# Optimization experiments

Measured on AMD Instinct MI355X. Metric: run time of the kernel, lower is better.

Reference implementation:

```python
import jax, jax.numpy as jnp
import numpy as np

FEATURES = 8
MAX_LAG = 50
OMEGA, ALPHA, BETA = 0.05, 0.1, 0.85   # garch_params
NU = 4.0                               # Student-t dof (hardcoded in source)
W_ACL, W_GARCH = 10.0, 0.001           # loss_weights
LOG_2PI = float(np.log(2.0 * np.pi))


def setup_inputs() -> dict:
    key = jax.random.key(0)
    k1, k2 = jax.random.split(key)
    x_true = jax.random.normal(k1, (4096, 512, FEATURES), dtype=jnp.float32)
    dec_out = jax.random.normal(k2, (4096, 512, 2 * FEATURES), dtype=jnp.float32)
    return {"x_true": x_true, "dec_out": dec_out}


def _series(y_pred):
    # concat(seq 0 full series, last value of every other sequence) -> [T + B - 1]
    return jnp.concatenate([y_pred[0, :, 0], y_pred[1:, -1, 0]], axis=0)


def _acl_loss(y_pred):
    s = _series(y_pred)
    n = s.shape[0]
    sc = s - jnp.mean(s)
    fft_len = 2 * n
    F = jnp.fft.rfft(sc, n=fft_len)
    autocorr = jnp.fft.irfft(jnp.conj(F) * F, n=fft_len)  # real by construction
    variance = jnp.sum(jnp.square(sc))
    autocorr = autocorr[: MAX_LAG + 1] / variance
    return jnp.mean(jnp.square(autocorr[1:]))


def _garch_nll_loss(y_pred):
    s = _series(y_pred)
    r = s - jnp.mean(s)
    r2 = jnp.square(r)
    sigma0 = OMEGA / (1.0 - ALPHA - BETA)  # unconditional variance

    def step(prev_sigma_sq, cur_r2):
        new = OMEGA + ALPHA * cur_r2 + BETA * prev_sigma_sq
        return new, new

    _, cond_var = jax.lax.scan(step, sigma0, r2)
    scale = jnp.sqrt(cond_var * (NU - 2.0) / NU)
    z = r / scale
    # StudentT(df=NU, loc=0, scale).log_prob(r)
    lp = (jax.scipy.special.gammaln((NU + 1.0) / 2.0)
          - jax.scipy.special.gammaln(NU / 2.0)
          - 0.5 * jnp.log(NU * jnp.pi)
          - jnp.log(scale)
          - (NU + 1.0) / 2.0 * jnp.log1p(z * z / NU))
    return -jnp.sum(lp)


def _gaussian_nll(x_true, dec_out):
    mean = dec_out[..., :FEATURES]
    log_var = dec_out[..., FEATURES:]
    ll = -0.5 * (LOG_2PI + log_var + jnp.square(x_true - mean) * jnp.exp(-log_var))
    return -jnp.mean(jnp.sum(ll, axis=(1, 2)))


def reference(x_true, dec_out):
    y_pred = dec_out[..., :FEATURES]  # generated_x = decoder means
    recon = _gaussian_nll(x_true, dec_out)
    acl = _acl_loss(y_pred)
    garch = _garch_nll_loss(y_pred)
    return recon + W_ACL * acl + W_GARCH * garch
```

## Files before the change

### kernel.cpp

```cpp
#include <hip/hip_runtime.h>

#define NS        4607
#define NBLK1     8192
#define N_TOTAL   16777216.0

#define WS_PART   0
#define WS_SRAW   8192
#define WS_GARCH  (8192 + NS)
#define WS_ACLSUM (8192 + NS + 1)
#define WS_CNT    (8192 + NS + 2)

__device__ __forceinline__ float wave_sum(float v) {
    for (int o = 32; o > 0; o >>= 1) v += __shfl_down(v, o);
    return v;
}

__global__ __launch_bounds__(256) void recon_kernel(
    const float* __restrict__ x, const float* __restrict__ dec,
    float* __restrict__ ws)
{
    const int tid = threadIdx.x;
    const long long pixBase = (long long)blockIdx.x * 256;
    const float4* dec4 = (const float4*)(dec + pixBase * 16);
    const float4* x4   = (const float4*)(x + pixBase * 8);

    float4 dv[4], xv[4];
#pragma unroll
    for (int r = 0; r < 4; ++r) {
        const int w = tid + r * 256;
        dv[r] = dec4[w];
        const int u = ((w >> 2) << 1) | (w & 1);
        xv[r] = x4[u];
    }

    float acc = 0.f;
#pragma unroll
    for (int r = 0; r < 4; ++r) {
        const int w = tid + r * 256;
        const int q = w & 3;
        float4 a = dv[r], b;
        b.x = __shfl_xor(a.x, 2);
        b.y = __shfl_xor(a.y, 2);
        b.z = __shfl_xor(a.z, 2);
        b.w = __shfl_xor(a.w, 2);
        const bool im = (q < 2);
        float4 m, lv;
        m.x  = im ? a.x : b.x;  m.y  = im ? a.y : b.y;
        m.z  = im ? a.z : b.z;  m.w  = im ? a.w : b.w;
        lv.x = im ? b.x : a.x;  lv.y = im ? b.y : a.y;
        lv.z = im ? b.z : a.z;  lv.w = im ? b.w : a.w;
        float4 xx = xv[r];
        float d;
        d = xx.x - m.x; acc += lv.x + d * d * __expf(-lv.x);
        d = xx.y - m.y; acc += lv.y + d * d * __expf(-lv.y);
        d = xx.z - m.z; acc += lv.z + d * d * __expf(-lv.z);
        d = xx.w - m.w; acc += lv.w + d * d * __expf(-lv.w);

        if (q == 0) {
            const long long pix = pixBase + (w >> 2);
            if (pix < 512)               ws[WS_SRAW + (int)pix] = m.x;
            else if ((pix & 511) == 511) ws[WS_SRAW + (int)(pix >> 9) + 511] = m.x;
        }
    }

    acc = wave_sum(acc);
    __shared__ float s4[4];
    if ((tid & 63) == 0) s4[tid >> 6] = acc;
    __syncthreads();
    if (tid == 0) {
        ws[WS_PART + blockIdx.x] = 0.5f * (s4[0] + s4[1] + s4[2] + s4[3]);
        if (blockIdx.x == 0) {
            ws[WS_GARCH]  = 0.f;
            ws[WS_ACLSUM] = 0.f;
            ((int*)ws)[WS_CNT] = 0;
        }
    }
}

__global__ __launch_bounds__(256) void tail_kernel(float* __restrict__ ws,
                                                   float* __restrict__ out)
{
    const float OMEGA = 0.05f, ALPHA = 0.1f, BETA = 0.85f;
    const int tid  = threadIdx.x;
    const int lane = tid & 63;
    const int wv   = tid >> 6;

    __shared__ float sc[NS];
    __shared__ float s4[4];
    __shared__ int   isLast;

    float lsum = 0.f;
    for (int j = tid; j < NS; j += 256) { float v = ws[WS_SRAW + j]; sc[j] = v; lsum += v; }
    lsum = wave_sum(lsum);
    __syncthreads();
    if (lane == 0) s4[wv] = lsum;
    __syncthreads();
    const float mean = (s4[0] + s4[1] + s4[2] + s4[3]) / (float)NS;

    float vsum = 0.f;
    __syncthreads();
    for (int j = tid; j < NS; j += 256) { float v = sc[j] - mean; sc[j] = v; vsum += v * v; }
    vsum = wave_sum(vsum);
    __syncthreads();
    if (lane == 0) s4[wv] = vsum;
    __syncthreads();
    const float var = s4[0] + s4[1] + s4[2] + s4[3];

    if (blockIdx.x == 0) {
        const int start = tid * 18;
        const int end   = min(start + 18, NS);
        float e = 0.f, p = 1.f;
        for (int i = start; i < end; ++i) {
            float r2 = sc[i] * sc[i];
            e = (OMEGA + ALPHA * r2) + BETA * e;
            p *= BETA;
        }
        for (int o = 1; o < 64; o <<= 1) {
            float pe = __shfl_up(e, o), pp = __shfl_up(p, o);
            if (lane >= o) { e = e + p * pe; p = p * pp; }
        }
        __shared__ float wE[4], wP[4];
        if (lane == 63) { wE[wv] = e; wP[wv] = p; }
        __syncthreads();
        float cE = 0.f, cP = 1.f;
        for (int t = 0; t < wv; ++t) { cE = wE[t] + wP[t] * cE; cP = wP[t] * cP; }
        float eE = __shfl_up(e, 1), eP = __shfl_up(p, 1);
        if (lane == 0) { eE = 0.f; eP = 1.f; }
        float prev = (eE + eP * cE) + (eP * cP) * 1.0f;
        float g = 0.f;
        for (int i = start; i < end; ++i) {
            float r2 = sc[i] * sc[i];
            float cv = OMEGA + ALPHA * r2 + BETA * prev;
            prev = cv;
            g += 0.5f * logf(0.5f * cv) + 2.5f * log1pf(r2 / (2.f * cv));
        }
        g = wave_sum(g);
        __syncthreads();
        if (lane == 0) s4[wv] = g;
        __syncthreads();
        if (tid == 0) atomicAdd(&ws[WS_GARCH], s4[0] + s4[1] + s4[2] + s4[3]);
    } else {
        const int k = blockIdx.x;
        float a = 0.f;
        for (int i = tid; i < NS - k; i += 256) a += sc[i] * sc[i + k];
        a = wave_sum(a);
        __syncthreads();
        if (lane == 0) s4[wv] = a;
        __syncthreads();
        if (tid == 0) {
            float r = (s4[0] + s4[1] + s4[2] + s4[3]) / var;
            atomicAdd(&ws[WS_ACLSUM], r * r);
        }
    }

    __syncthreads();
    if (tid == 0) {
        __threadfence();
        isLast = (atomicAdd((int*)ws + WS_CNT, 1) == 50) ? 1 : 0;
    }
    __syncthreads();
    if (isLast) {
        __threadfence();
        __shared__ double d4[4];
        double ds = 0.0;
        for (int i = tid; i < NBLK1; i += 256) ds += (double)ws[WS_PART + i];
        for (int o = 32; o > 0; o >>= 1) ds += __shfl_down(ds, o);
        if (lane == 0) d4[wv] = ds;
        __syncthreads();
        if (tid == 0) {
            float garch_f = atomicAdd(&ws[WS_GARCH], 0.f);
            float acl_f   = atomicAdd(&ws[WS_ACLSUM], 0.f);
            const double LOG_2PI = 1.8378770664093453;
            const double NEG_C   = 0.9808292530117262;
            double q = d4[0] + d4[1] + d4[2] + d4[3];
            double recon = 0.5 * (q + N_TOTAL * LOG_2PI) / 4096.0;
            double acl   = (double)acl_f / 50.0;
            double garch = (double)garch_f + (double)NS * NEG_C;
            out[0] = (float)(recon + 10.0 * acl + 0.001 * garch);
        }
    }
}

extern "C" void kernel_launch(void* const* d_in, const int* in_sizes, int n_in,
                              void* d_out, int out_size, void* d_ws, size_t ws_size,
                              hipStream_t stream) {
    const float* x_true  = (const float*)d_in[0];
    const float* dec_out = (const float*)d_in[1];
    float* ws  = (float*)d_ws;
    float* out = (float*)d_out;

    recon_kernel<<<NBLK1, 256, 0, stream>>>(x_true, dec_out, ws);
    tail_kernel<<<51, 256, 0, stream>>>(ws, out);
}
```

Before: 251.4 us.

## Overlap ACL/GARCH tail work with recon blocks in one merged kernel

Merges the serial tail blocks (autocorrelation lags and GARCH scan) into the recon kernel as the first 51 blocks. These blocks read the series values straight from dec_out, so they run alongside the bandwidth-bound recon reduction instead of after it. A small single-block final kernel then combines the per-block partials, replacing the atomic counter and last-block pattern. The cost is that each of the 51 tail blocks does strided gathers from global memory and uses large shared memory, which can reduce occupancy early in the grid.

```diff
diff --git a/kernel.cpp b/kernel.cpp
--- a/kernel.cpp
+++ b/kernel.cpp
@@ -1,183 +1,176 @@
 #include <hip/hip_runtime.h>
 
 #define NS        4607
-#define NBLK1     8192
+#define NRECON    8192
+#define NTAIL     51
 #define N_TOTAL   16777216.0
 
 #define WS_PART   0
-#define WS_SRAW   8192
-#define WS_GARCH  (8192 + NS)
-#define WS_ACLSUM (8192 + NS + 1)
-#define WS_CNT    (8192 + NS + 2)
+#define WS_GARCH  8192
+#define WS_ACL    8193
 
 __device__ __forceinline__ float wave_sum(float v) {
     for (int o = 32; o > 0; o >>= 1) v += __shfl_down(v, o);
     return v;
 }
 
-__global__ __launch_bounds__(256) void recon_kernel(
+__global__ __launch_bounds__(256) void main_kernel(
     const float* __restrict__ x, const float* __restrict__ dec,
     float* __restrict__ ws)
 {
-    const int tid = threadIdx.x;
-    const long long pixBase = (long long)blockIdx.x * 256;
-    const float4* dec4 = (const float4*)(dec + pixBase * 16);
-    const float4* x4   = (const float4*)(x + pixBase * 8);
+    const int tid  = threadIdx.x;
+    const int lane = tid & 63;
+    const int wv   = tid >> 6;
 
-    float4 dv[4], xv[4];
+    if (blockIdx.x >= NTAIL) {
+        const int tile = blockIdx.x - NTAIL;
+        const long long pixBase = (long long)tile * 256;
+        const float4* dec4 = (const float4*)(dec + pixBase * 16);
+        const float4* x4   = (const float4*)(x + pixBase * 8);
+
+        float4 dv[4], xv[4];
 #pragma unroll
-    for (int r = 0; r < 4; ++r) {
-        const int w = tid + r * 256;
-        dv[r] = dec4[w];
-        const int u = ((w >> 2) << 1) | (w & 1);
-        xv[r] = x4[u];
-    }
+        for (int r = 0; r < 4; ++r) {
+            const int w = tid + r * 256;
+            dv[r] = dec4[w];
+            const int u = ((w >> 2) << 1) | (w & 1);
+            xv[r] = x4[u];
+        }
 
-    float acc = 0.f;
+        float acc = 0.f;
 #pragma unroll
-    for (int r = 0; r < 4; ++r) {
-        const int w = tid + r * 256;
-        const int q = w & 3;
-        float4 a = dv[r], b;
-        b.x = __shfl_xor(a.x, 2);
-        b.y = __shfl_xor(a.y, 2);
-        b.z = __shfl_xor(a.z, 2);
-        b.w = __shfl_xor(a.w, 2);
-        const bool im = (q < 2);
-        float4 m, lv;
-        m.x  = im ? a.x : b.x;  m.y  = im ? a.y : b.y;
-        m.z  = im ? a.z : b.z;  m.w  = im ? a.w : b.w;
-        lv.x = im ? b.x : a.x;  lv.y = im ? b.y : a.y;
-        lv.z = im ? b.z : a.z;  lv.w = im ? b.w : a.w;
-        float4 xx = xv[r];
-        float d;
-        d = xx.x - m.x; acc += lv.x + d * d * __expf(-lv.x);
-        d = xx.y - m.y; acc += lv.y + d * d * __expf(-lv.y);
-        d = xx.z - m.z; acc += lv.z + d * d * __expf(-lv.z);
-        d = xx.w - m.w; acc += lv.w + d * d * __expf(-lv.w);
+        for (int r = 0; r < 4; ++r) {
+            const int w = tid + r * 256;
+            const int q = w & 3;
+            float4 a = dv[r], b;
+            b.x = __shfl_xor(a.x, 2);
+            b.y = __shfl_xor(a.y, 2);
+            b.z = __shfl_xor(a.z, 2);
+            b.w = __shfl_xor(a.w, 2);
+            const bool im = (q < 2);
+            float4 m, lv;
+            m.x  = im ? a.x : b.x;  m.y  = im ? a.y : b.y;
+            m.z  = im ? a.z : b.z;  m.w  = im ? a.w : b.w;
+            lv.x = im ? b.x : a.x;  lv.y = im ? b.y : a.y;
+            lv.z = im ? b.z : a.z;  lv.w = im ? b.w : a.w;
+            float4 xx = xv[r];
+            float d;
+            d = xx.x - m.x; acc += lv.x + d * d * __expf(-lv.x);
+            d = xx.y - m.y; acc += lv.y + d * d * __expf(-lv.y);
+            d = xx.z - m.z; acc += lv.z + d * d * __expf(-lv.z);
+            d = xx.w - m.w; acc += lv.w + d * d * __expf(-lv.w);
+        }
 
-        if (q == 0) {
-            const long long pix = pixBase + (w >> 2);
-            if (pix < 512)               ws[WS_SRAW + (int)pix] = m.x;
-            else if ((pix & 511) == 511) ws[WS_SRAW + (int)(pix >> 9) + 511] = m.x;
+        acc = wave_sum(acc);
+        __shared__ float p4[4];
+        if (lane == 0) p4[wv] = acc;
+        __syncthreads();
+        if (tid == 0) ws[WS_PART + tile] = 0.5f * (p4[0] + p4[1] + p4[2] + p4[3]);
+    } else {
+        const float OMEGA = 0.05f, ALPHA = 0.1f, BETA = 0.85f;
+        __shared__ float sc[NS];
+        __shared__ float s4[4];
+
+        float lsum = 0.f;
+        for (int j = tid; j < NS; j += 256) {
+            float v = (j < 512) ? dec[(long long)j * 16]
+                                : dec[(long long)(j - 511) * 8192 + 8176];
+            sc[j] = v;
+            lsum += v;
         }
-    }
+        lsum = wave_sum(lsum);
+        __syncthreads();
+        if (lane == 0) s4[wv] = lsum;
+        __syncthreads();
+        const float mean = (s4[0] + s4[1] + s4[2] + s4[3]) / (float)NS;
 
-    acc = wave_sum(acc);
-    __shared__ float s4[4];
-    if ((tid & 63) == 0) s4[tid >> 6] = acc;
-    __syncthreads();
-    if (tid == 0) {
-        ws[WS_PART + blockIdx.x] = 0.5f * (s4[0] + s4[1] + s4[2] + s4[3]);
+        float vsum = 0.f;
+        __syncthreads();
+        for (int j = tid; j < NS; j += 256) { float v = sc[j] - mean; sc[j] = v; vsum += v * v; }
+        vsum = wave_sum(vsum);
+        __syncthreads();
+        if (lane == 0) s4[wv] = vsum;
+        __syncthreads();
+        const float var = s4[0] + s4[1] + s4[2] + s4[3];
+
         if (blockIdx.x == 0) {
-            ws[WS_GARCH]  = 0.f;
-            ws[WS_ACLSUM] = 0.f;
-            ((int*)ws)[WS_CNT] = 0;
+            const int start = tid * 18;
+            const int end   = min(start + 18, NS);
+            float e = 0.f, p = 1.f;
+            for (int i = start; i < end; ++i) {
+                float r2 = sc[i] * sc[i];
+                e = (OMEGA + ALPHA * r2) + BETA * e;
+                p *= BETA;
+            }
+            for (int o = 1; o < 64; o <<= 1) {
+                float pe = __shfl_up(e, o), pp = __shfl_up(p, o);
+                if (lane >= o) { e = e + p * pe; p = p * pp; }
+            }
+            __shared__ float wE[4], wP[4];
+            if (lane == 63) { wE[wv] = e; wP[wv] = p; }
+            __syncthreads();
+            float cE = 0.f, cP = 1.f;
+            for (int t = 0; t < wv; ++t) { cE = wE[t] + wP[t] * cE; cP = wP[t] * cP; }
+            float eE = __shfl_up(e, 1), eP = __shfl_up(p, 1);
+            if (lane == 0) { eE = 0.f; eP = 1.f; }
+            float prev = (eE + eP * cE) + (eP * cP) * 1.0f;
+            float g = 0.f;
+            for (int i = start; i < end; ++i) {
+                float r2 = sc[i] * sc[i];
+                float cv = OMEGA + ALPHA * r2 + BETA * prev;
+                prev = cv;
+                g += 0.5f * logf(0.5f * cv) + 2.5f * log1pf(r2 / (2.f * cv));
+            }
+            g = wave_sum(g);
+            __syncthreads();
+            if (lane == 0) s4[wv] = g;
+            __syncthreads();
+            if (tid == 0) ws[WS_GARCH] = s4[0] + s4[1] + s4[2] + s4[3];
+        } else {
+            const int k = blockIdx.x;
+            float a = 0.f;
+            for (int i = tid; i < NS - k; i += 256) a += sc[i] * sc[i + k];
+            a = wave_sum(a);
+            __syncthreads();
+            if (lane == 0) s4[wv] = a;
+            __syncthreads();
+            if (tid == 0) {
+                float r = (s4[0] + s4[1] + s4[2] + s4[3]) / var;
+                ws[WS_ACL + (k - 1)] = r * r;
+            }
         }
     }
 }
 
-__global__ __launch_bounds__(256) void tail_kernel(float* __restrict__ ws,
-                                                   float* __restrict__ out)
+__global__ __launch_bounds__(256) void final_kernel(
+    const float* __restrict__ ws, float* __restrict__ out)
 {
-    const float OMEGA = 0.05f, ALPHA = 0.1f, BETA = 0.85f;
     const int tid  = threadIdx.x;
     const int lane = tid & 63;
     const int wv   = tid >> 6;
+    __shared__ double d4[4];
+    __shared__ float  aclbuf[1];
 
-    __shared__ float sc[NS];
-    __shared__ float s4[4];
-    __shared__ int   isLast;
+    double ds = 0.0;
+    for (int i = tid; i < NRECON; i += 256) ds += (double)ws[WS_PART + i];
+    for (int o = 32; o > 0; o >>= 1) ds += __shfl_down(ds, o);
+    if (lane == 0) d4[wv] = ds;
 
-    float lsum = 0.f;
-    for (int j = tid; j < NS; j += 256) { float v = ws[WS_SRAW + j]; sc[j] = v; lsum += v; }
-    lsum = wave_sum(lsum);
-    __syncthreads();
-    if (lane == 0) s4[wv] = lsum;
-    __syncthreads();
-    const float mean = (s4[0] + s4[1] + s4[2] + s4[3]) / (float)NS;
-
-    float vsum = 0.f;
-    __syncthreads();
-    for (int j = tid; j < NS; j += 256) { float v = sc[j] - mean; sc[j] = v; vsum += v * v; }
-    vsum = wave_sum(vsum);
-    __syncthreads();
-    if (lane == 0) s4[wv] = vsum;
-    __syncthreads();
-    const float var = s4[0] + s4[1] + s4[2] + s4[3];
-
-    if (blockIdx.x == 0) {
-        const int start = tid * 18;
-        const int end   = min(start + 18, NS);
-        float e = 0.f, p = 1.f;
-        for (int i = start; i < end; ++i) {
-            float r2 = sc[i] * sc[i];
-            e = (OMEGA + ALPHA * r2) + BETA * e;
-            p *= BETA;
-        }
-        for (int o = 1; o < 64; o <<= 1) {
-            float pe = __shfl_up(e, o), pp = __shfl_up(p, o);
-            if (lane >= o) { e = e + p * pe; p = p * pp; }
-        }
-        __shared__ float wE[4], wP[4];
-        if (lane == 63) { wE[wv] = e; wP[wv] = p; }
-        __syncthreads();
-        float cE = 0.f, cP = 1.f;
-        for (int t = 0; t < wv; ++t) { cE = wE[t] + wP[t] * cE; cP = wP[t] * cP; }
-        float eE = __shfl_up(e, 1), eP = __shfl_up(p, 1);
-        if (lane == 0) { eE = 0.f; eP = 1.f; }
-        float prev = (eE + eP * cE) + (eP * cP) * 1.0f;
-        float g = 0.f;
-        for (int i = start; i < end; ++i) {
-            float r2 = sc[i] * sc[i];
-            float cv = OMEGA + ALPHA * r2 + BETA * prev;
-            prev = cv;
-            g += 0.5f * logf(0.5f * cv) + 2.5f * log1pf(r2 / (2.f * cv));
-        }
-        g = wave_sum(g);
-        __syncthreads();
-        if (lane == 0) s4[wv] = g;
-        __syncthreads();
-        if (tid == 0) atomicAdd(&ws[WS_GARCH], s4[0] + s4[1] + s4[2] + s4[3]);
-    } else {
-        const int k = blockIdx.x;
-        float a = 0.f;
-        for (int i = tid; i < NS - k; i += 256) a += sc[i] * sc[i + k];
-        a = wave_sum(a);
-        __syncthreads();
-        if (lane == 0) s4[wv] = a;
-        __syncthreads();
-        if (tid == 0) {
-            float r = (s4[0] + s4[1] + s4[2] + s4[3]) / var;
-            atomicAdd(&ws[WS_ACLSUM], r * r);
-        }
-    }
-
-    __syncthreads();
-    if (tid == 0) {
-        __threadfence();
-        isLast = (atomicAdd((int*)ws + WS_CNT, 1) == 50) ? 1 : 0;
+    if (wv == 0) {
+        float av = (lane < 50) ? ws[WS_ACL + lane] : 0.f;
+        av = wave_sum(av);
+        if (lane == 0) aclbuf[0] = av;
     }
     __syncthreads();
-    if (isLast) {
-        __threadfence();
-        __shared__ double d4[4];
-        double ds = 0.0;
-        for (int i = tid; i < NBLK1; i += 256) ds += (double)ws[WS_PART + i];
-        for (int o = 32; o > 0; o >>= 1) ds += __shfl_down(ds, o);
-        if (lane == 0) d4[wv] = ds;
-        __syncthreads();
-        if (tid == 0) {
-            float garch_f = atomicAdd(&ws[WS_GARCH], 0.f);
-            float acl_f   = atomicAdd(&ws[WS_ACLSUM], 0.f);
-            const double LOG_2PI = 1.8378770664093453;
-            const double NEG_C   = 0.9808292530117262;
-            double q = d4[0] + d4[1] + d4[2] + d4[3];
-            double recon = 0.5 * (q + N_TOTAL * LOG_2PI) / 4096.0;
-            double acl   = (double)acl_f / 50.0;
-            double garch = (double)garch_f + (double)NS * NEG_C;
-            out[0] = (float)(recon + 10.0 * acl + 0.001 * garch);
-        }
+
+    if (tid == 0) {
+        const double LOG_2PI = 1.8378770664093453;
+        const double NEG_C   = 0.9808292530117262;
+        double q = d4[0] + d4[1] + d4[2] + d4[3];
+        double recon = 0.5 * (q + N_TOTAL * LOG_2PI) / 4096.0;
+        double acl   = (double)aclbuf[0] / 50.0;
+        double garch = (double)ws[WS_GARCH] + (double)NS * NEG_C;
+        out[0] = (float)(recon + 10.0 * acl + 0.001 * garch);
     }
 }
 
@@ -189,6 +182,6 @@
     float* ws  = (float*)d_ws;
     float* out = (float*)d_out;
 
-    recon_kernel<<<NBLK1, 256, 0, stream>>>(x_true, dec_out, ws);
-    tail_kernel<<<51, 256, 0, stream>>>(ws, out);
+    main_kernel<<<NRECON + NTAIL, 256, 0, stream>>>(x_true, dec_out, ws);
+    final_kernel<<<1, 256, 0, stream>>>(ws, out);
 }
```

After: 246.1 us. 1.02x faster.
